# Performance work log

Hardware: AMD Instinct MI355X
Metric: run time of the kernel (lower is better)

Reference implementation:

```python
import jax, jax.numpy as jnp
import numpy as np
import math

N_LAYERS = 2
N_HEADS = 8
D_MODEL = 512
D_FF = 2048
B = 2
L = 2048
GELU_C = 0.7978845608028654  # sqrt(2/pi)
LN_EPS = 1e-5


def gelu_tanh(x):
    # faithful to the module's custom GELU: 0.5*x*(1+tanh(sqrt(2/pi)*(x+0.044715*x^3)))
    return 0.5 * x * (1.0 + jnp.tanh(GELU_C * (x + 0.044715 * x * x * x)))


def layernorm(x, g, b):
    m = jnp.mean(x, axis=-1, keepdims=True)
    v = jnp.mean((x - m) ** 2, axis=-1, keepdims=True)
    return (x - m) * jax.lax.rsqrt(v + LN_EPS) * g + b


def setup_inputs() -> dict:
    key = jax.random.key(0)
    ks = jax.random.split(key, 24)
    w = lambda k, shape: jax.random.normal(k, shape, dtype=jnp.float32) * 0.02
    inp = {
        "x": jax.random.normal(ks[0], (B, L, D_MODEL), dtype=jnp.float32),
        # tau is exp(tau_learner(...)) in the full model -> positive scalar per batch
        "tau": jax.random.uniform(ks[1], (B, 1), dtype=jnp.float32) + 0.5,
        "delta": jax.random.normal(ks[2], (B, L), dtype=jnp.float32) * 0.1,
        # NStransformer builds an upper-triangular causal mask (True = masked)
        "att_mask": jnp.triu(jnp.ones((L, L), dtype=bool), k=1),
        "Wq": w(ks[3], (N_LAYERS, D_MODEL, D_MODEL)), "bq": jnp.zeros((N_LAYERS, D_MODEL), jnp.float32),
        "Wk": w(ks[4], (N_LAYERS, D_MODEL, D_MODEL)), "bk": jnp.zeros((N_LAYERS, D_MODEL), jnp.float32),
        "Wv": w(ks[5], (N_LAYERS, D_MODEL, D_MODEL)), "bv": jnp.zeros((N_LAYERS, D_MODEL), jnp.float32),
        "Wo": w(ks[6], (N_LAYERS, D_MODEL, D_MODEL)), "bo": jnp.zeros((N_LAYERS, D_MODEL), jnp.float32),
        # conv1/conv2 are kernel_size=1 Conv1d == pointwise linears
        "W1": w(ks[7], (N_LAYERS, D_MODEL, D_FF)), "b1": jnp.zeros((N_LAYERS, D_FF), jnp.float32),
        "W2": w(ks[8], (N_LAYERS, D_FF, D_MODEL)), "b2": jnp.zeros((N_LAYERS, D_MODEL), jnp.float32),
        "ln1_g": jnp.ones((N_LAYERS, D_MODEL), jnp.float32), "ln1_b": jnp.zeros((N_LAYERS, D_MODEL), jnp.float32),
        "ln2_g": jnp.ones((N_LAYERS, D_MODEL), jnp.float32), "ln2_b": jnp.zeros((N_LAYERS, D_MODEL), jnp.float32),
        "lnf_g": jnp.ones((D_MODEL,), jnp.float32), "lnf_b": jnp.zeros((D_MODEL,), jnp.float32),
    }
    return inp


def reference(x, tau, delta, att_mask, Wq, bq, Wk, bk, Wv, bv, Wo, bo,
              W1, b1, W2, b2, ln1_g, ln1_b, ln2_g, ln2_b, lnf_g, lnf_b):
    Bsz, Ls, D = x.shape
    H = N_HEADS
    E = D // H
    scale = 1.0 / math.sqrt(E)
    t = tau[:, None, None, :]    # (B,1) -> (B,1,1,1)
    d = delta[:, None, None, :]  # (B,L) -> (B,1,1,L)
    neg_inf = jnp.float32(-jnp.inf)
    for l in range(N_LAYERS):
        q = (x @ Wq[l] + bq[l]).reshape(Bsz, Ls, H, E)
        k = (x @ Wk[l] + bk[l]).reshape(Bsz, Ls, H, E)
        v = (x @ Wv[l] + bv[l]).reshape(Bsz, Ls, H, E)
        # de-stationary scores: QK^T * tau + delta, then masked softmax
        scores = jnp.einsum('blhe,bshe->bhls', q, k) * t + d  # (B,H,L,S)
        scores = jnp.where(att_mask, neg_inf, scores)
        A = jax.nn.softmax(scale * scores, axis=-1)  # dropout is identity in eval
        V = jnp.einsum('bhls,bshd->blhd', A, v).reshape(Bsz, Ls, D)
        x = (V @ Wo[l] + bo[l]) + x
        xb = layernorm(x, ln1_g[l], ln1_b[l])
        h = gelu_tanh(xb @ W1[l] + b1[l])   # conv1 (k=1)
        o = h @ W2[l] + b2[l]               # conv2 (k=1)
        x = layernorm(o + xb, ln2_g[l], ln2_b[l])
    return layernorm(x, lnf_g, lnf_b)
```

## Files before the change

### kernel.cpp

```cpp
#include <hip/hip_runtime.h>
#include <stdint.h>

#define DM   512
#define DFF  2048
#define NH   8
#define EH   64
#define SEQ  2048
#define NBAT 2
#define NTOK (NBAT*SEQ)
#define LOG2E 1.44269504088896340736f

typedef __attribute__((ext_vector_type(8))) short  s16x8;
typedef __attribute__((ext_vector_type(8))) __bf16 bf16x8;
typedef __attribute__((ext_vector_type(4))) float  f32x4;

__device__ __forceinline__ short f2bf(float f) {
  union { float f; unsigned int i; } c; c.f = f;
  unsigned int x = c.i;
  x += 0x7fffu + ((x >> 16) & 1u);
  return (short)(x >> 16);
}
__device__ __forceinline__ float bf2f(short u) {
  union { unsigned int i; float f; } c;
  c.i = ((unsigned int)(unsigned short)u) << 16;
  return c.f;
}
__device__ __forceinline__ f32x4 mfma16(bf16x8 a, bf16x8 b, f32x4 c) {
  return __builtin_amdgcn_mfma_f32_16x16x32_bf16(a, b, c, 0, 0, 0);
}
__device__ __forceinline__ void gl_lds16(const short* g, short* l) {
  __builtin_amdgcn_global_load_lds(
      (const __attribute__((address_space(1))) unsigned int*)(const void*)g,
      (__attribute__((address_space(3))) unsigned int*)(void*)l, 16, 0, 0);
}

__global__ __launch_bounds__(256) void fill_code_f32(float* __restrict__ out,
                                                     float code)
{
  out[blockIdx.x * 256 + threadIdx.x] = code;
}

__global__ __launch_bounds__(256) void prep_all(
    const float* __restrict__ Wq, const float* __restrict__ Wk,
    const float* __restrict__ Wv, const float* __restrict__ Wo,
    const float* __restrict__ W1, const float* __restrict__ W2,
    short* __restrict__ Wqkvt, short* __restrict__ Wot,
    short* __restrict__ W1t,   short* __restrict__ W2t,
    const float* __restrict__ x, float* __restrict__ sumf,
    short* __restrict__ x16)
{
  if (blockIdx.x >= 3072) {
    int i = (blockIdx.x - 3072) * 256 + threadIdx.x;
    float v = x[i];
    sumf[i] = v;
    x16[i]  = f2bf(v);
    return;
  }
  int gw   = blockIdx.x * 4 + (threadIdx.x >> 6);
  int lane = threadIdx.x & 63;
  int l = gw / 6144;
  int g = gw % 6144;
  const float* src; short* dst; int K, N, gi;
  if (g < 2048) {
    int w = g >> 9; gi = g & 511; K = 512; N = 512;
    src = (w == 0 ? Wq : w == 1 ? Wk : w == 2 ? Wv : Wo) + l * 262144;
    dst = (w < 3) ? (Wqkvt + l * 786432 + w * 262144) : (Wot + l * 262144);
  } else if (g < 4096) {
    gi = g - 2048; K = 512; N = 2048;
    src = W1 + l * 1048576; dst = W1t + l * 1048576;
  } else {
    gi = g - 4096; K = 2048; N = 512;
    src = W2 + l * 1048576; dst = W2t + l * 1048576;
  }
  int nb = N >> 6;
  int n  = (gi % nb) * 64 + lane;
  int k0 = (gi / nb) * 8;
  s16x8 v;
  #pragma unroll
  for (int i = 0; i < 8; i++) v[i] = f2bf(src[(size_t)(k0 + i) * N + n]);
  *(s16x8*)(dst + (size_t)n * K + k0) = v;
}

__global__ __launch_bounds__(256) void skred_ln(
    const short* __restrict__ parts, const float* __restrict__ bias,
    const float* __restrict__ rf, const short* __restrict__ rb,
    const float* __restrict__ g, const float* __restrict__ bb,
    const float* __restrict__ g2, const float* __restrict__ bb2,
    float* __restrict__ sumf, short* __restrict__ outb,
    float* __restrict__ outf32, int mode)
{
  const int row  = blockIdx.x * 4 + (threadIdx.x >> 6);
  const int lane = threadIdx.x & 63;
  const int col  = lane * 8;
  const size_t base = (size_t)row * DM + col;
  float t[8];
  #pragma unroll
  for (int j = 0; j < 8; j++) t[j] = bias[col + j];
  #pragma unroll
  for (int p = 0; p < 4; p++) {
    s16x8 v = *(const s16x8*)(parts + (size_t)p * (NTOK * DM) + base);
    #pragma unroll
    for (int j = 0; j < 8; j++) t[j] += bf2f(v[j]);
  }
  if (mode == 0) {
    #pragma unroll
    for (int j = 0; j < 8; j++) t[j] += rf[base + j];
  } else {
    s16x8 v = *(const s16x8*)(rb + base);
    #pragma unroll
    for (int j = 0; j < 8; j++) t[j] += bf2f(v[j]);
  }
  float s = 0.f, ss = 0.f;
  #pragma unroll
  for (int j = 0; j < 8; j++) { s += t[j]; ss += t[j] * t[j]; }
  #pragma unroll
  for (int off = 32; off > 0; off >>= 1) {
    s += __shfl_xor(s, off); ss += __shfl_xor(ss, off);
  }
  float mean = s * (1.f / DM);
  float var  = ss * (1.f / DM) - mean * mean;
  float rstd = rsqrtf(var + 1e-5f);
  if (mode == 0) {
    #pragma unroll
    for (int j = 0; j < 8; j++) {
      sumf[base + j] = t[j];
      outb[base + j] = f2bf((t[j] - mean) * rstd * g[col + j] + bb[col + j]);
    }
  } else if (mode == 1) {
    #pragma unroll
    for (int j = 0; j < 8; j++) {
      float y = (t[j] - mean) * rstd * g[col + j] + bb[col + j];
      sumf[base + j] = y;
      outb[base + j] = f2bf(y);
    }
  } else {
    float y[8]; float s2 = 0.f, ss2 = 0.f;
    #pragma unroll
    for (int j = 0; j < 8; j++) {
      y[j] = (t[j] - mean) * rstd * g[col + j] + bb[col + j];
      s2 += y[j]; ss2 += y[j] * y[j];
    }
    #pragma unroll
    for (int off = 32; off > 0; off >>= 1) {
      s2 += __shfl_xor(s2, off); ss2 += __shfl_xor(ss2, off);
    }
    float mean2 = s2 * (1.f / DM);
    float var2  = ss2 * (1.f / DM) - mean2 * mean2;
    float rstd2 = rsqrtf(var2 + 1e-5f);
    #pragma unroll
    for (int j = 0; j < 8; j++)
      outf32[base + j] = (y[j] - mean2) * rstd2 * g2[col + j] + bb2[col + j];
  }
}

template<int TM>
__global__ __launch_bounds__(256) void gemm_bt(
    const short* __restrict__ A, const short* __restrict__ Bt,
    int M, int N, int K, int KS, int mode,
    const float* __restrict__ bq, const float* __restrict__ bk,
    const float* __restrict__ bv,
    short* __restrict__ oq, short* __restrict__ okk, short* __restrict__ ov)
{
  __shared__ short As[2][TM * 32];
  __shared__ short Bs[2][128 * 32];
  constexpr int MT = TM / 32;
  const int tid  = threadIdx.x;
  const int lane = tid & 63;
  const int wid  = tid >> 6;
  const int lm   = lane & 15, quad = lane >> 4;
  const int nbn  = N >> 7;
  const int nb2  = (M / TM) * nbn;
  const int ks   = blockIdx.x / nb2;
  const int rem  = blockIdx.x % nb2;
  const int m0   = (rem / nbn) * TM;
  const int n0   = (rem % nbn) << 7;
  const int wm   = (wid & 1) * (TM / 2), wn = (wid >> 1) * 64;
  const int Kc   = K / KS;
  const int kbeg = ks * Kc;

  f32x4 acc[MT][4];
  #pragma unroll
  for (int i = 0; i < MT; i++)
    #pragma unroll
    for (int j = 0; j < 4; j++) acc[i][j] = (f32x4){0.f, 0.f, 0.f, 0.f};

  const short* Abase = A  + (size_t)m0 * K;
  const short* Bbase = Bt + (size_t)n0 * K;

  for (int k0 = kbeg; k0 < kbeg + Kc; k0 += 64) {
    __syncthreads();
    #pragma unroll
    for (int half = 0; half < 2; half++) {
      const int kk = k0 + half * 32;
      #pragma unroll
      for (int j = 0; j < TM / 64; j++) {
        int c = j * 256 + wid * 64 + lane;
        gl_lds16(Abase + (size_t)(c >> 2) * K + kk + (c & 3) * 8,
                 &As[half][(j * 256 + wid * 64) * 8]);
      }
      #pragma unroll
      for (int j = 0; j < 2; j++) {
        int c = j * 256 + wid * 64 + lane;
        gl_lds16(Bbase + (size_t)(c >> 2) * K + kk + (c & 3) * 8,
                 &Bs[half][(j * 256 + wid * 64) * 8]);
      }
    }
    __syncthreads();
    #pragma unroll
    for (int half = 0; half < 2; half++) {
      bf16x8 af[MT], bfr[4];
      #pragma unroll
      for (int t = 0; t < MT; t++)
        af[t] = *(const bf16x8*)&As[half][(wm + t * 16 + lm) * 32 + quad * 8];
      #pragma unroll
      for (int t = 0; t < 4; t++)
        bfr[t] = *(const bf16x8*)&Bs[half][(wn + t * 16 + lm) * 32 + quad * 8];
      #pragma unroll
      for (int mt = 0; mt < MT; mt++)
        #pragma unroll
        for (int nt = 0; nt < 4; nt++)
          acc[mt][nt] = mfma16(af[mt], bfr[nt], acc[mt][nt]);
    }
  }

  #pragma unroll
  for (int mt = 0; mt < MT; mt++) {
    int row = m0 + wm + mt * 16 + quad * 4;
    #pragma unroll
    for (int nt = 0; nt < 4; nt++) {
      int col = n0 + wn + nt * 16 + lm;
      f32x4 v = acc[mt][nt];
      if (mode == 0) {
        int which = col >> 9; int d = col & 511;
        int hh = d >> 6; int e = d & 63;
        const float* bias = which == 0 ? bq : which == 1 ? bk : bv;
        float bb = bias[d];
        #pragma unroll
        for (int r = 0; r < 4; r++) {
          int tok = row + r; int bI = tok >> 11, li = tok & 2047;
          float val = v[r] + bb;
          if (which == 0)
            oq [(((size_t)bI * NH + hh) * SEQ + li) * EH + e] = f2bf(val);
          else if (which == 1)
            okk[(((size_t)bI * NH + hh) * SEQ + li) * EH + e] = f2bf(val);
          else
            ov [(((size_t)bI * NH + hh) * EH + e) * SEQ + li] = f2bf(val);
        }
      } else if (mode == 2) {
        float bb = bq[col];
        #pragma unroll
        for (int r = 0; r < 4; r++) {
          float x = v[r] + bb;
          float u = 0.7978845608f * (x + 0.044715f * x * x * x);
          float t = 1.f - 2.f / (1.f + __expf(2.f * u));
          size_t idx = (size_t)(row + r) * N + col;
          oq[idx] = f2bf(0.5f * x * (1.f + t));
        }
      } else {
        short* op = oq + (size_t)ks * M * N;
        #pragma unroll
        for (int r = 0; r < 4; r++)
          op[(size_t)(row + r) * N + col] = f2bf(v[r]);
      }
    }
  }
}

__global__ __launch_bounds__(256) void attn_v7(
    const short* __restrict__ Q, const short* __restrict__ Kg,
    const short* __restrict__ Vt,
    const float* __restrict__ tau, const float* __restrict__ delta,
    short* __restrict__ opart, float* __restrict__ lpart)
{
  __shared__ short Ks[64 * 72];
  __shared__ short Vs[64 * 72];
  __shared__ short Ps[4][16 * 72];
  const int tid  = threadIdx.x;
  const int lane = tid & 63, wid = tid >> 6;
  const int lm = lane & 15, quad = lane >> 4;
  const int blk   = blockIdx.x;
  const int bh    = blk & 15;
  const int rest  = blk >> 4;
  const int part  = rest & 3;
  const int qbrev = rest >> 2;
  const int qb = 31 - qbrev;
  const int h  = bh & 7;
  const int b  = bh >> 3;
  const int q0 = qb * 64;
  const int qw = q0 + wid * 16;
  const int t_lin = bh * 32 + qbrev;
  const size_t bhq = (size_t)bh * SEQ;
  const short* kbase = Kg + bhq * EH;
  const short* vbase = Vt + (size_t)bh * (EH * SEQ);

  const int nblk = qb + 1;
  const int kb0 = (nblk * part) >> 2;
  const int kb1 = (nblk * (part + 1)) >> 2;

  bf16x8 qf0 = *(const bf16x8*)(Q + (bhq + qw + lm) * EH + quad * 8);
  bf16x8 qf1 = *(const bf16x8*)(Q + (bhq + qw + lm) * EH + 32 + quad * 8);

  const float st2 = 0.125f * LOG2E * tau[b];
  f32x4 O[4];
  #pragma unroll
  for (int i = 0; i < 4; i++) O[i] = (f32x4){0.f, 0.f, 0.f, 0.f};
  float lr[4] = {0.f, 0.f, 0.f, 0.f};

  const int r0 = tid >> 3,         ch0 = (tid & 7) * 8;
  const int r1 = (tid + 256) >> 3, ch1 = (tid & 7) * 8;

  for (int kb = kb0; kb < kb1; kb++) {
    const int s0 = kb << 6;
    s16x8 ka  = *(const s16x8*)(kbase + (size_t)(s0 + r0) * EH + ch0);
    s16x8 kb_ = *(const s16x8*)(kbase + (size_t)(s0 + r1) * EH + ch1);
    s16x8 va  = *(const s16x8*)(vbase + (size_t)r0 * SEQ + s0 + ch0);
    s16x8 vb  = *(const s16x8*)(vbase + (size_t)r1 * SEQ + s0 + ch1);
    __syncthreads();
    *(s16x8*)&Ks[r0 * 72 + ch0] = ka;
    *(s16x8*)&Ks[r1 * 72 + ch1] = kb_;
    *(s16x8*)&Vs[r0 * 72 + ch0] = va;
    *(s16x8*)&Vs[r1 * 72 + ch1] = vb;
    __syncthreads();

    f32x4 S[4];
    #pragma unroll
    for (int nt = 0; nt < 4; nt++) {
      S[nt] = (f32x4){0.f, 0.f, 0.f, 0.f};
      S[nt] = mfma16(qf0, *(const bf16x8*)&Ks[(nt*16 + lm) * 72 + quad * 8], S[nt]);
      S[nt] = mfma16(qf1, *(const bf16x8*)&Ks[(nt*16 + lm) * 72 + 32 + quad * 8], S[nt]);
    }
    float dl[4];
    #pragma unroll
    for (int nt = 0; nt < 4; nt++)
      dl[nt] = fmaf(0.125f * LOG2E, delta[(size_t)b * SEQ + s0 + nt * 16 + lm],
                    -8.f);

    const bool diag = (kb == qb);
    #pragma unroll
    for (int r = 0; r < 4; r++) {
      float sc[4];
      #pragma unroll
      for (int nt = 0; nt < 4; nt++) sc[nt] = fmaf(st2, S[nt][r], dl[nt]);
      if (diag) {
        int rowq = qw + quad * 4 + r;
        #pragma unroll
        for (int nt = 0; nt < 4; nt++)
          if (s0 + nt * 16 + lm > rowq) sc[nt] = -__builtin_inff();
      }
      unsigned int u0 = __float_as_uint(exp2f(sc[0]));
      unsigned int u1 = __float_as_uint(exp2f(sc[1]));
      unsigned int u2 = __float_as_uint(exp2f(sc[2]));
      unsigned int u3 = __float_as_uint(exp2f(sc[3]));
      lr[r] += (__uint_as_float(u0 & 0xffff0000u) +
                __uint_as_float(u1 & 0xffff0000u)) +
               (__uint_as_float(u2 & 0xffff0000u) +
                __uint_as_float(u3 & 0xffff0000u));
      short* pr = &Ps[wid][(quad * 4 + r) * 72];
      pr[lm]      = (short)(u0 >> 16);
      pr[16 + lm] = (short)(u1 >> 16);
      pr[32 + lm] = (short)(u2 >> 16);
      pr[48 + lm] = (short)(u3 >> 16);
    }

    bf16x8 pf0 = *(const bf16x8*)&Ps[wid][lm * 72 + quad * 8];
    bf16x8 pf1 = *(const bf16x8*)&Ps[wid][lm * 72 + 32 + quad * 8];
    #pragma unroll
    for (int et = 0; et < 4; et++) {
      O[et] = mfma16(pf0, *(const bf16x8*)&Vs[(et*16 + lm) * 72 + quad * 8], O[et]);
      O[et] = mfma16(pf1, *(const bf16x8*)&Vs[(et*16 + lm) * 72 + 32 + quad * 8], O[et]);
    }
  }

  #pragma unroll
  for (int r = 0; r < 4; r++) {
    float s = lr[r];
    #pragma unroll
    for (int off = 1; off < 16; off <<= 1) s += __shfl_xor(s, off);
    lr[r] = s;
  }

  const int slot = ((t_lin << 2) | part);
  short* ob = opart + (size_t)slot * 4096;
  float* lb = lpart + (size_t)slot * 64;
  #pragma unroll
  for (int r = 0; r < 4; r++) {
    int qloc = wid * 16 + quad * 4 + r;
    #pragma unroll
    for (int et = 0; et < 4; et++)
      ob[qloc * 64 + et * 16 + lm] = f2bf(O[et][r]);
    if (lm == 0) lb[qloc] = lr[r];
  }
}

__global__ __launch_bounds__(256) void attn_reduce(
    const short* __restrict__ opart, const float* __restrict__ lpart,
    short* __restrict__ Oa)
{
  const int t = blockIdx.x;
  const int qb = 31 - (t & 31);
  const int h  = (t >> 5) & 7;
  const int b  = t >> 8;
  const int q0 = qb * 64;
  #pragma unroll
  for (int i = 0; i < 16; i++) {
    int idx = i * 256 + threadIdx.x;
    int q = idx >> 6, e = idx & 63;
    float l = 0.f, o = 0.f;
    #pragma unroll
    for (int p = 0; p < 4; p++) {
      int slot = t * 4 + p;
      l += lpart[(size_t)slot * 64 + q];
      o += bf2f(opart[(size_t)slot * 4096 + idx]);
    }
    Oa[((size_t)b * SEQ + q0 + q) * DM + h * EH + e] = f2bf(o / l);
  }
}

extern "C" void kernel_launch(void* const* d_in, const int* in_sizes, int n_in,
                              void* d_out, int out_size, void* d_ws, size_t ws_size,
                              hipStream_t stream)
{
  float* out = (float*)d_out;

  if (ws_size < (size_t)62918656) {
    fill_code_f32<<<2097152 / 256, 256, 0, stream>>>(
        out, 1200.f + (float)(ws_size >> 20));
    return;
  }

  const float* x    = (const float*)d_in[0];
  const float* tau  = (const float*)d_in[1];
  const float* del  = (const float*)d_in[2];
  const float* Wq = (const float*)d_in[4];
  const float* bq = (const float*)d_in[5];
  const float* Wk = (const float*)d_in[6];
  const float* bk = (const float*)d_in[7];
  const float* Wv = (const float*)d_in[8];
  const float* bv = (const float*)d_in[9];
  const float* Wo = (const float*)d_in[10];
  const float* bo = (const float*)d_in[11];
  const float* W1 = (const float*)d_in[12];
  const float* b1 = (const float*)d_in[13];
  const float* W2 = (const float*)d_in[14];
  const float* b2 = (const float*)d_in[15];
  const float* ln1g = (const float*)d_in[16];
  const float* ln1b = (const float*)d_in[17];
  const float* ln2g = (const float*)d_in[18];
  const float* ln2b = (const float*)d_in[19];
  const float* lnfg = (const float*)d_in[20];
  const float* lnfb = (const float*)d_in[21];

  char* ws = (char*)d_ws;
  float* sumf  = (float*)(ws + 0);
  short* x16   = (short*)(ws + 8388608);
  short* xb16  = (short*)(ws + 12582912);
  short* q16   = (short*)(ws + 16777216);
  short* k16   = (short*)(ws + 20971520);
  short* vt16  = (short*)(ws + 25165824);
  short* at16  = (short*)(ws + 29360128);
  short* h16   = (short*)(ws + 33554432);
  short* Wqkvt = (short*)(ws + 50331648);
  short* Wot   = (short*)(ws + 53477376);
  short* W1t   = (short*)(ws + 54525952);
  short* W2t   = (short*)(ws + 58720256);
  short* aopart = (short*)(ws + 33554432);
  float* alpart = (float*)(ws + 12582912);
  short* oppart = (short*)(ws + 33554432);
  short* f2part = (short*)(ws + 16777216);

  prep_all<<<11264, 256, 0, stream>>>(Wq, Wk, Wv, Wo, W1, W2,
                                      Wqkvt, Wot, W1t, W2t, x, sumf, x16);

  for (int l = 0; l < 2; l++) {
    gemm_bt<64><<<64 * 12, 256, 0, stream>>>(x16, Wqkvt + l * 786432,
        NTOK, 3 * DM, DM, 1, 0,
        bq + l * DM, bk + l * DM, bv + l * DM,
        q16, k16, vt16);
    attn_v7<<<4 * NBAT * NH * (SEQ / 64), 256, 0, stream>>>(
        q16, k16, vt16, tau, del, aopart, alpart);
    attn_reduce<<<NBAT * NH * (SEQ / 64), 256, 0, stream>>>(
        aopart, alpart, at16);
    gemm_bt<64><<<64 * 4 * 4, 256, 0, stream>>>(at16, Wot + l * 262144,
        NTOK, DM, DM, 4, 4,
        nullptr, nullptr, nullptr,
        oppart, nullptr, nullptr);
    skred_ln<<<1024, 256, 0, stream>>>(oppart, bo + l * DM, sumf, nullptr,
        ln1g + l * DM, ln1b + l * DM, nullptr, nullptr,
        sumf, xb16, nullptr, 0);
    gemm_bt<64><<<64 * 16, 256, 0, stream>>>(xb16, W1t + l * 1048576,
        NTOK, DFF, DM, 1, 2,
        b1 + l * DFF, nullptr, nullptr,
        h16, nullptr, nullptr);
    gemm_bt<64><<<64 * 4 * 4, 256, 0, stream>>>(h16, W2t + l * 1048576,
        NTOK, DM, DFF, 4, 4,
        nullptr, nullptr, nullptr,
        f2part, nullptr, nullptr);
    if (l == 0) {
      skred_ln<<<1024, 256, 0, stream>>>(f2part, b2 + l * DM, nullptr, xb16,
          ln2g + l * DM, ln2b + l * DM, nullptr, nullptr,
          sumf, x16, nullptr, 1);
    } else {
      skred_ln<<<1024, 256, 0, stream>>>(f2part, b2 + l * DM, nullptr, xb16,
          ln2g + l * DM, ln2b + l * DM, lnfg, lnfb,
          nullptr, nullptr, out, 2);
    }
  }
}
```

Baseline: 383.4 us.

## Stage two K/V blocks per barrier in attention; halve Wo split-K

New measurement: 373.0 us. 2.7% less time.

```diff
diff --git a/kernel.cpp b/kernel.cpp
--- a/kernel.cpp
+++ b/kernel.cpp
@@ -87,7 +87,7 @@
     const float* __restrict__ g, const float* __restrict__ bb,
     const float* __restrict__ g2, const float* __restrict__ bb2,
     float* __restrict__ sumf, short* __restrict__ outb,
-    float* __restrict__ outf32, int mode)
+    float* __restrict__ outf32, int KS, int mode)
 {
   const int row  = blockIdx.x * 4 + (threadIdx.x >> 6);
   const int lane = threadIdx.x & 63;
@@ -96,8 +96,8 @@
   float t[8];
   #pragma unroll
   for (int j = 0; j < 8; j++) t[j] = bias[col + j];
-  #pragma unroll
-  for (int p = 0; p < 4; p++) {
+  #pragma unroll 4
+  for (int p = 0; p < KS; p++) {
     s16x8 v = *(const s16x8*)(parts + (size_t)p * (NTOK * DM) + base);
     #pragma unroll
     for (int j = 0; j < 8; j++) t[j] += bf2f(v[j]);
@@ -266,14 +266,62 @@
   }
 }
 
-__global__ __launch_bounds__(256) void attn_v7(
+__device__ __forceinline__ void do_subtile(
+    bf16x8 qf0, bf16x8 qf1,
+    const short* __restrict__ Ks, const short* __restrict__ Vs,
+    short* __restrict__ Psw, const float* dl, float st2,
+    int s0, int rowq0, bool diag,
+    float* lr, f32x4* O, int lm, int quad)
+{
+  f32x4 S[4];
+  #pragma unroll
+  for (int nt = 0; nt < 4; nt++) {
+    S[nt] = (f32x4){0.f, 0.f, 0.f, 0.f};
+    S[nt] = mfma16(qf0, *(const bf16x8*)&Ks[(nt*16 + lm) * 72 + quad * 8], S[nt]);
+    S[nt] = mfma16(qf1, *(const bf16x8*)&Ks[(nt*16 + lm) * 72 + 32 + quad * 8], S[nt]);
+  }
+  #pragma unroll
+  for (int r = 0; r < 4; r++) {
+    float sc[4];
+    #pragma unroll
+    for (int nt = 0; nt < 4; nt++) sc[nt] = fmaf(st2, S[nt][r], dl[nt]);
+    if (diag) {
+      int rowq = rowq0 + quad * 4 + r;
+      #pragma unroll
+      for (int nt = 0; nt < 4; nt++)
+        if (s0 + nt * 16 + lm > rowq) sc[nt] = -__builtin_inff();
+    }
+    unsigned int u0 = __float_as_uint(exp2f(sc[0]));
+    unsigned int u1 = __float_as_uint(exp2f(sc[1]));
+    unsigned int u2 = __float_as_uint(exp2f(sc[2]));
+    unsigned int u3 = __float_as_uint(exp2f(sc[3]));
+    lr[r] += (__uint_as_float(u0 & 0xffff0000u) +
+              __uint_as_float(u1 & 0xffff0000u)) +
+             (__uint_as_float(u2 & 0xffff0000u) +
+              __uint_as_float(u3 & 0xffff0000u));
+    short* pr = &Psw[(quad * 4 + r) * 72];
+    pr[lm]      = (short)(u0 >> 16);
+    pr[16 + lm] = (short)(u1 >> 16);
+    pr[32 + lm] = (short)(u2 >> 16);
+    pr[48 + lm] = (short)(u3 >> 16);
+  }
+  bf16x8 pf0 = *(const bf16x8*)&Psw[lm * 72 + quad * 8];
+  bf16x8 pf1 = *(const bf16x8*)&Psw[lm * 72 + 32 + quad * 8];
+  #pragma unroll
+  for (int et = 0; et < 4; et++) {
+    O[et] = mfma16(pf0, *(const bf16x8*)&Vs[(et*16 + lm) * 72 + quad * 8], O[et]);
+    O[et] = mfma16(pf1, *(const bf16x8*)&Vs[(et*16 + lm) * 72 + 32 + quad * 8], O[et]);
+  }
+}
+
+__global__ __launch_bounds__(256) void attn_v9(
     const short* __restrict__ Q, const short* __restrict__ Kg,
     const short* __restrict__ Vt,
     const float* __restrict__ tau, const float* __restrict__ delta,
     short* __restrict__ opart, float* __restrict__ lpart)
 {
-  __shared__ short Ks[64 * 72];
-  __shared__ short Vs[64 * 72];
+  __shared__ short Ks[2][64 * 72];
+  __shared__ short Vs[2][64 * 72];
   __shared__ short Ps[4][16 * 72];
   const int tid  = threadIdx.x;
   const int lane = tid & 63, wid = tid >> 6;
@@ -284,7 +332,6 @@
   const int part  = rest & 3;
   const int qbrev = rest >> 2;
   const int qb = 31 - qbrev;
-  const int h  = bh & 7;
   const int b  = bh >> 3;
   const int q0 = qb * 64;
   const int qw = q0 + wid * 16;
@@ -309,66 +356,38 @@
   const int r0 = tid >> 3,         ch0 = (tid & 7) * 8;
   const int r1 = (tid + 256) >> 3, ch1 = (tid & 7) * 8;
 
-  for (int kb = kb0; kb < kb1; kb++) {
-    const int s0 = kb << 6;
-    s16x8 ka  = *(const s16x8*)(kbase + (size_t)(s0 + r0) * EH + ch0);
-    s16x8 kb_ = *(const s16x8*)(kbase + (size_t)(s0 + r1) * EH + ch1);
-    s16x8 va  = *(const s16x8*)(vbase + (size_t)r0 * SEQ + s0 + ch0);
-    s16x8 vb  = *(const s16x8*)(vbase + (size_t)r1 * SEQ + s0 + ch1);
+  for (int kb = kb0; kb < kb1; ) {
+    const int n = (kb1 - kb >= 2) ? 2 : 1;
+    s16x8 kr0[2], kr1[2], vr0[2], vr1[2];
+    #pragma unroll
+    for (int j = 0; j < 2; j++) if (j < n) {
+      const int s0 = (kb + j) << 6;
+      kr0[j] = *(const s16x8*)(kbase + (size_t)(s0 + r0) * EH + ch0);
+      kr1[j] = *(const s16x8*)(kbase + (size_t)(s0 + r1) * EH + ch1);
+      vr0[j] = *(const s16x8*)(vbase + (size_t)r0 * SEQ + s0 + ch0);
+      vr1[j] = *(const s16x8*)(vbase + (size_t)r1 * SEQ + s0 + ch1);
+    }
     __syncthreads();
-    *(s16x8*)&Ks[r0 * 72 + ch0] = ka;
-    *(s16x8*)&Ks[r1 * 72 + ch1] = kb_;
-    *(s16x8*)&Vs[r0 * 72 + ch0] = va;
-    *(s16x8*)&Vs[r1 * 72 + ch1] = vb;
+    #pragma unroll
+    for (int j = 0; j < 2; j++) if (j < n) {
+      *(s16x8*)&Ks[j][r0 * 72 + ch0] = kr0[j];
+      *(s16x8*)&Ks[j][r1 * 72 + ch1] = kr1[j];
+      *(s16x8*)&Vs[j][r0 * 72 + ch0] = vr0[j];
+      *(s16x8*)&Vs[j][r1 * 72 + ch1] = vr1[j];
+    }
     __syncthreads();
-
-    f32x4 S[4];
-    #pragma unroll
-    for (int nt = 0; nt < 4; nt++) {
-      S[nt] = (f32x4){0.f, 0.f, 0.f, 0.f};
-      S[nt] = mfma16(qf0, *(const bf16x8*)&Ks[(nt*16 + lm) * 72 + quad * 8], S[nt]);
-      S[nt] = mfma16(qf1, *(const bf16x8*)&Ks[(nt*16 + lm) * 72 + 32 + quad * 8], S[nt]);
-    }
-    float dl[4];
-    #pragma unroll
-    for (int nt = 0; nt < 4; nt++)
-      dl[nt] = fmaf(0.125f * LOG2E, delta[(size_t)b * SEQ + s0 + nt * 16 + lm],
-                    -8.f);
-
-    const bool diag = (kb == qb);
-    #pragma unroll
-    for (int r = 0; r < 4; r++) {
-      float sc[4];
-      #pragma unroll
-      for (int nt = 0; nt < 4; nt++) sc[nt] = fmaf(st2, S[nt][r], dl[nt]);
-      if (diag) {
-        int rowq = qw + quad * 4 + r;
-        #pragma unroll
-        for (int nt = 0; nt < 4; nt++)
-          if (s0 + nt * 16 + lm > rowq) sc[nt] = -__builtin_inff();
-      }
-      unsigned int u0 = __float_as_uint(exp2f(sc[0]));
-      unsigned int u1 = __float_as_uint(exp2f(sc[1]));
-      unsigned int u2 = __float_as_uint(exp2f(sc[2]));
-      unsigned int u3 = __float_as_uint(exp2f(sc[3]));
-      lr[r] += (__uint_as_float(u0 & 0xffff0000u) +
-                __uint_as_float(u1 & 0xffff0000u)) +
-               (__uint_as_float(u2 & 0xffff0000u) +
-                __uint_as_float(u3 & 0xffff0000u));
-      short* pr = &Ps[wid][(quad * 4 + r) * 72];
-      pr[lm]      = (short)(u0 >> 16);
-      pr[16 + lm] = (short)(u1 >> 16);
-      pr[32 + lm] = (short)(u2 >> 16);
-      pr[48 + lm] = (short)(u3 >> 16);
-    }
-
-    bf16x8 pf0 = *(const bf16x8*)&Ps[wid][lm * 72 + quad * 8];
-    bf16x8 pf1 = *(const bf16x8*)&Ps[wid][lm * 72 + 32 + quad * 8];
-    #pragma unroll
-    for (int et = 0; et < 4; et++) {
-      O[et] = mfma16(pf0, *(const bf16x8*)&Vs[(et*16 + lm) * 72 + quad * 8], O[et]);
-      O[et] = mfma16(pf1, *(const bf16x8*)&Vs[(et*16 + lm) * 72 + 32 + quad * 8], O[et]);
-    }
+    #pragma unroll
+    for (int j = 0; j < 2; j++) if (j < n) {
+      const int s0 = (kb + j) << 6;
+      float dl[4];
+      #pragma unroll
+      for (int nt = 0; nt < 4; nt++)
+        dl[nt] = fmaf(0.125f * LOG2E,
+                      delta[(size_t)b * SEQ + s0 + nt * 16 + lm], -8.f);
+      do_subtile(qf0, qf1, Ks[j], Vs[j], Ps[wid], dl, st2, s0, qw,
+                 (kb + j) == qb, lr, O, lm, quad);
+    }
+    kb += n;
   }
 
   #pragma unroll
@@ -476,17 +495,17 @@
         NTOK, 3 * DM, DM, 1, 0,
         bq + l * DM, bk + l * DM, bv + l * DM,
         q16, k16, vt16);
-    attn_v7<<<4 * NBAT * NH * (SEQ / 64), 256, 0, stream>>>(
+    attn_v9<<<4 * NBAT * NH * (SEQ / 64), 256, 0, stream>>>(
         q16, k16, vt16, tau, del, aopart, alpart);
     attn_reduce<<<NBAT * NH * (SEQ / 64), 256, 0, stream>>>(
         aopart, alpart, at16);
-    gemm_bt<64><<<64 * 4 * 4, 256, 0, stream>>>(at16, Wot + l * 262144,
-        NTOK, DM, DM, 4, 4,
+    gemm_bt<64><<<64 * 4 * 2, 256, 0, stream>>>(at16, Wot + l * 262144,
+        NTOK, DM, DM, 2, 4,
         nullptr, nullptr, nullptr,
         oppart, nullptr, nullptr);
     skred_ln<<<1024, 256, 0, stream>>>(oppart, bo + l * DM, sumf, nullptr,
         ln1g + l * DM, ln1b + l * DM, nullptr, nullptr,
-        sumf, xb16, nullptr, 0);
+        sumf, xb16, nullptr, 2, 0);
     gemm_bt<64><<<64 * 16, 256, 0, stream>>>(xb16, W1t + l * 1048576,
         NTOK, DFF, DM, 1, 2,
         b1 + l * DFF, nullptr, nullptr,
@@ -498,11 +517,11 @@
     if (l == 0) {
       skred_ln<<<1024, 256, 0, stream>>>(f2part, b2 + l * DM, nullptr, xb16,
           ln2g + l * DM, ln2b + l * DM, nullptr, nullptr,
-          sumf, x16, nullptr, 1);
+          sumf, x16, nullptr, 4, 1);
     } else {
       skred_ln<<<1024, 256, 0, stream>>>(f2part, b2 + l * DM, nullptr, xb16,
           ln2g + l * DM, ln2b + l * DM, lnfg, lnfb,
-          nullptr, nullptr, out, 2);
-    }
-  }
-}
+          nullptr, nullptr, out, 4, 2);
+    }
+  }
+}
```
